# Performance work log

Measured on AMD Instinct MI355X. Metric: run time of the kernel, lower is better.

The kernel has to match this reference:

```python
import jax, jax.numpy as jnp
import numpy as np

B, Z, OUT, NODES = 2048, 64, 512, 64
TRIPLES = 3 * (NODES - 1)  # (self, left, right) per real node
EPS_BN = 1e-5
EPS_TLN = 1e-5
SLOPE = 0.01  # LeakyReLU default


def setup_inputs() -> dict:
    key = jax.random.key(0)
    ks = jax.random.split(key, 12)
    def n(k, shape, s=0.05):
        return jax.random.normal(k, shape, jnp.float32) * s
    inp = {
        "trees": jax.random.normal(ks[0], (B, Z), jnp.float32),
        "indexes": jax.random.randint(ks[1], (B, TRIPLES, 1), 0, NODES),
        # MLP: Linear(Z,64) -> BN -> Linear(64,256) -> BN -> Linear(256,1024) -> BN -> Linear(1024,4096) -> BN
        "w1": n(ks[2], (64, Z)),      "b1": jnp.zeros((64,), jnp.float32),
        "g1": jnp.ones((64,), jnp.float32),   "be1": jnp.zeros((64,), jnp.float32),
        "w2": n(ks[3], (256, 64)),    "b2": jnp.zeros((256,), jnp.float32),
        "g2": jnp.ones((256,), jnp.float32),  "be2": jnp.zeros((256,), jnp.float32),
        "w3": n(ks[4], (1024, 256)),  "b3": jnp.zeros((1024,), jnp.float32),
        "g3": jnp.ones((1024,), jnp.float32), "be3": jnp.zeros((1024,), jnp.float32),
        "w4": n(ks[5], (4096, 1024)), "b4": jnp.zeros((4096,), jnp.float32),
        "g4": jnp.ones((4096,), jnp.float32), "be4": jnp.zeros((4096,), jnp.float32),
        # BinaryTreeConv weights: Conv1d(in,out,kernel=3,stride=3) -> (out,in,3)
        "cw1": n(ks[6], (128, 64, 3)),  "cb1": jnp.zeros((128,), jnp.float32),
        "cw2": n(ks[7], (256, 128, 3)), "cb2": jnp.zeros((256,), jnp.float32),
        "cw3": n(ks[8], (OUT, 256, 3)), "cb3": jnp.zeros((OUT,), jnp.float32),
    }
    return inp


def _bn(x, g, b):
    # BatchNorm1d in training mode: batch statistics, biased variance
    m = jnp.mean(x, axis=0)
    v = jnp.var(x, axis=0)
    return g * (x - m) * jax.lax.rsqrt(v + EPS_BN) + b


def _lrelu(x):
    return jnp.where(x > 0, x, SLOPE * x)


def _tree_conv(x, idx, w, b):
    # x: (B, C, N); idx: (B, 3M) node indices; w: (O, C, 3)
    Bn, C, _ = x.shape
    expanded = jnp.take_along_axis(x, idx[:, None, :], axis=2)  # (B, C, 3M) gather
    expanded = expanded.reshape(Bn, C, -1, 3)                    # (B, C, M, 3)
    out = jnp.einsum('bcmk,ock->bom', expanded, w) + b[None, :, None]
    zero = jnp.zeros((Bn, w.shape[0], 1), x.dtype)               # re-attach null-node slot
    return jnp.concatenate([zero, out], axis=2)                  # (B, O, M+1)


def _tree_norm(x):
    # TreeLayerNorm: normalize over (channels, nodes) per sample; torch.std is unbiased
    m = jnp.mean(x, axis=(1, 2), keepdims=True)
    s = jnp.std(x, axis=(1, 2), ddof=1, keepdims=True)
    return (x - m) / (s + EPS_TLN)


def reference(trees, indexes, w1, b1, g1, be1, w2, b2, g2, be2, w3, b3, g3, be3,
              w4, b4, g4, be4, cw1, cb1, cw2, cb2, cw3, cb3):
    idx = indexes[..., 0]  # (B, 3M)
    h = _lrelu(_bn(trees @ w1.T + b1, g1, be1))
    h = _lrelu(_bn(h @ w2.T + b2, g2, be2))
    h = _lrelu(_bn(h @ w3.T + b3, g3, be3))
    h = _lrelu(_bn(h @ w4.T + b4, g4, be4))
    x = h.reshape(h.shape[0], 64, 64)  # (B, C=64, N=64)
    x = _lrelu(_tree_norm(_tree_conv(x, idx, cw1, cb1)))
    x = _lrelu(_tree_norm(_tree_conv(x, idx, cw2, cb2)))
    x = _lrelu(_tree_norm(_tree_conv(x, idx, cw3, cb3)))
    return x  # (B, OUT, 64)
```

## Files before the change

kernel.cpp:

```cpp
#include <hip/hip_runtime.h>

typedef unsigned short u16;
typedef unsigned int   u32;
typedef __attribute__((ext_vector_type(8))) short short8;
typedef __attribute__((ext_vector_type(4))) float f32x4;
typedef __attribute__((ext_vector_type(4))) u16  u16x4;

#define DI __device__ __forceinline__

DI float b2f(u16 v){ return __builtin_bit_cast(float, (u32)v << 16); }
DI u16 f2b(float f){ u32 u = __builtin_bit_cast(u32, f); return (u16)((u + 0x7fffu + ((u >> 16) & 1u)) >> 16); }
DI float lrelu(float v){ return v > 0.f ? v : 0.01f * v; }

__global__ __launch_bounds__(256)
void cvt_bf16(const float* __restrict__ in, u16* __restrict__ out, int n4)
{
  int i = blockIdx.x*256 + threadIdx.x;
  if (i >= n4) return;
  float4 v = ((const float4*)in)[i];
  u16x4 o; o[0]=f2b(v.x); o[1]=f2b(v.y); o[2]=f2b(v.z); o[3]=f2b(v.w);
  *(u16x4*)(out + (size_t)i*4) = o;
}

template<int BM, int BN, int WROWS, int WCOLS, int RT, int CT, bool APPLY>
__global__ __launch_bounds__(WROWS*WCOLS*64)
void gemm_bn(const float* __restrict__ A, const u16* __restrict__ W,
             const float* __restrict__ ssA,
             float* __restrict__ Y, float* __restrict__ part,
             int M, int N, int K)
{
  constexpr int NT  = WROWS*WCOLS*64;
  constexpr int ALD = (BM*4)/NT;
  constexpr int BLD = (BN*4)/NT;
  __shared__ __align__(16) u16 As[BM*32];
  __shared__ __align__(16) u16 Bs[BN*32];
  __shared__ float colS[WROWS][BN], colS2[WROWS][BN];
  const int tid  = threadIdx.x;
  const int wave = tid >> 6, lane = tid & 63;
  const int wr = wave / WCOLS, wc = wave % WCOLS;
  const int lrow = lane & 15, kg = lane >> 4;
  const int m0 = blockIdx.x * BM, n0 = blockIdx.y * BN;
  f32x4 acc[RT][CT] = {};
  for (int k0 = 0; k0 < K; k0 += 32) {
    uint4 av[ALD], bv[BLD];
#pragma unroll
    for (int i = 0; i < ALD; i++){
      int x = tid + i*NT; int kc = k0 + (x&3)*8;
      const float* ap = A + (size_t)(m0 + (x>>2))*K + kc;
      float4 y0 = *(const float4*)ap, y1 = *(const float4*)(ap + 4);
      float v[8] = {y0.x,y0.y,y0.z,y0.w,y1.x,y1.y,y1.z,y1.w};
      if constexpr (APPLY){
        float4 c0 = *(const float4*)(ssA + kc),     c1 = *(const float4*)(ssA + kc + 4);
        float4 h0 = *(const float4*)(ssA + K + kc), h1 = *(const float4*)(ssA + K + kc + 4);
        v[0]=lrelu(v[0]*c0.x+h0.x); v[1]=lrelu(v[1]*c0.y+h0.y);
        v[2]=lrelu(v[2]*c0.z+h0.z); v[3]=lrelu(v[3]*c0.w+h0.w);
        v[4]=lrelu(v[4]*c1.x+h1.x); v[5]=lrelu(v[5]*c1.y+h1.y);
        v[6]=lrelu(v[6]*c1.z+h1.z); v[7]=lrelu(v[7]*c1.w+h1.w);
      }
      u32 w0 = (u32)f2b(v[0]) | ((u32)f2b(v[1])<<16);
      u32 w1 = (u32)f2b(v[2]) | ((u32)f2b(v[3])<<16);
      u32 w2 = (u32)f2b(v[4]) | ((u32)f2b(v[5])<<16);
      u32 w3 = (u32)f2b(v[6]) | ((u32)f2b(v[7])<<16);
      av[i] = (uint4){w0,w1,w2,w3};
    }
#pragma unroll
    for (int i = 0; i < BLD; i++){ int x = tid + i*NT; bv[i] = *(const uint4*)(W + (size_t)(n0 + (x>>2))*K + k0 + (x&3)*8); }
    __syncthreads();
#pragma unroll
    for (int i = 0; i < ALD; i++){ *(uint4*)(As + (tid + i*NT)*8) = av[i]; }
#pragma unroll
    for (int i = 0; i < BLD; i++){ *(uint4*)(Bs + (tid + i*NT)*8) = bv[i]; }
    __syncthreads();
    short8 af[RT], bfr[CT];
#pragma unroll
    for (int r = 0; r < RT; r++) af[r]  = *(const short8*)(As + ((wr*RT + r)*16 + lrow)*32 + kg*8);
#pragma unroll
    for (int c = 0; c < CT; c++) bfr[c] = *(const short8*)(Bs + ((wc*CT + c)*16 + lrow)*32 + kg*8);
#pragma unroll
    for (int r = 0; r < RT; r++)
#pragma unroll
      for (int c = 0; c < CT; c++)
        acc[r][c] = __builtin_amdgcn_mfma_f32_16x16x32_bf16(af[r], bfr[c], acc[r][c], 0, 0, 0);
  }
#pragma unroll
  for (int r = 0; r < RT; r++)
#pragma unroll
    for (int c = 0; c < CT; c++)
#pragma unroll
      for (int i = 0; i < 4; i++){
        int m = m0 + (wr*RT + r)*16 + kg*4 + i;
        int n = n0 + (wc*CT + c)*16 + lrow;
        Y[(size_t)m*N + n] = acc[r][c][i];
      }
#pragma unroll
  for (int c = 0; c < CT; c++){
    float s = 0.f, s2 = 0.f;
#pragma unroll
    for (int r = 0; r < RT; r++)
#pragma unroll
      for (int i = 0; i < 4; i++){ float v = acc[r][c][i]; s += v; s2 += v*v; }
    s  += __shfl_xor(s, 16);  s  += __shfl_xor(s, 32);
    s2 += __shfl_xor(s2, 16); s2 += __shfl_xor(s2, 32);
    if (kg == 0){ colS[wr][(wc*CT + c)*16 + lrow] = s; colS2[wr][(wc*CT + c)*16 + lrow] = s2; }
  }
  __syncthreads();
  if (tid < BN){
    float S = 0.f, S2 = 0.f;
#pragma unroll
    for (int w = 0; w < WROWS; w++){ S += colS[w][tid]; S2 += colS2[w][tid]; }
    part[(size_t)(blockIdx.x*2+0)*N + n0 + tid] = S;
    part[(size_t)(blockIdx.x*2+1)*N + n0 + tid] = S2;
  }
}

__global__ __launch_bounds__(256)
void bn_finalize(const float* __restrict__ part, const float* __restrict__ g,
                 const float* __restrict__ be, float* __restrict__ ss, int N, int M, int split)
{
  int n = blockIdx.x*256 + threadIdx.x;
  if (n >= N) return;
  float s = 0.f, s2 = 0.f;
  for (int i = 0; i < split; i++){ s += part[(size_t)(i*2+0)*N + n]; s2 += part[(size_t)(i*2+1)*N + n]; }
  float inv  = 1.f / (float)M;
  float mean = s * inv;
  float var  = fmaxf(s2*inv - mean*mean, 0.f);
  float sc   = g[n] * rsqrtf(var + 1e-5f);
  ss[n]     = sc;
  ss[N + n] = be[n] - mean*sc;
}

__global__ __launch_bounds__(256)
void bn_apply4_t(const float* __restrict__ Y, const float* __restrict__ ss, u16* __restrict__ Xt)
{
  const int b = blockIdx.x, tid = threadIdx.x;
  __shared__ u16 t[64*65];
  for (int j = tid; j < 4096; j += 256){
    float v = Y[(size_t)b*4096 + j];
    v = lrelu(v*ss[j] + ss[4096 + j]);
    int c = j >> 6, n = j & 63;
    t[c*65 + n] = f2b(v);
  }
  __syncthreads();
  for (int e = tid; e < 4096; e += 256){
    int n = e >> 6, c = e & 63;
    Xt[(size_t)b*4096 + n*64 + c] = t[c*65 + n];
  }
}

__global__ __launch_bounds__(256)
void repack_w_frag(const float* __restrict__ w, u16* __restrict__ wr, int O, int C, int lgC)
{
  int e = blockIdx.x*256 + threadIdx.x;
  int R = 3*C;
  if (e >= O*R) return;
  int NK   = R >> 5;
  int j    = e & 7;
  int lane = (e >> 3) & 63;
  int blk  = e >> 9;
  int tr   = blk / NK, kb = blk - tr*NK;
  int row  = tr*16 + (lane & 15);
  int kcol = kb*32 + (lane >> 4)*8 + j;
  int k = kcol >> lgC; int c = kcol & (C-1);
  wr[e] = f2b(w[(size_t)row*R + c*3 + k]);
}

template<int C, int O, int WAVES, int MINW, bool PIPE, bool LAST>
__global__ __launch_bounds__(WAVES*64, MINW)
void conv_norm(const u16* __restrict__ Xin, const u16* __restrict__ Wr,
               const float* __restrict__ cb, const int* __restrict__ gidx,
               u16* __restrict__ Xout, float* __restrict__ Outf)
{
  constexpr int R    = 3*C;
  constexpr int NK   = R/32;
  constexpr int CSI  = C + 8;
  constexpr int RT   = O/(WAVES*16);
  constexpr int NT   = WAVES*64;
  constexpr int LGC  = (C==64)?6:((C==128)?7:8);
  constexpr int LG32 = LGC - 5;
  __shared__ __align__(16) u16 xs[65*CSI];
  __shared__ int idxs[192];
  __shared__ float red[2*WAVES];
  const int b = blockIdx.x, tid = threadIdx.x;
  const int wave = tid >> 6, lane = tid & 63;
  const int lrow = lane & 15, kg = lane >> 4;

  const u16* xg = Xin + (size_t)b*64*C;
  for (int e = tid; e < 64*(C/8); e += NT){
    int row = e/(C/8), t = e%(C/8);
    *(uint4*)(xs + row*CSI + t*8) = *(const uint4*)(xg + row*C + t*8);
  }
  for (int e = tid; e < C/8; e += NT){ uint4 z = {0,0,0,0}; *(uint4*)(xs + 64*CSI + e*8) = z; }
  if (tid < 189){ int v = gidx[b*189 + tid]; idxs[tid] = v & 63; }
  __syncthreads();

  int jr0[4], jr1[4], jr2[4];
#pragma unroll
  for (int ct = 0; ct < 4; ct++){
    int n = ct*16 + lrow;
    jr0[ct] = (n == 0) ? 64 : idxs[3*(n-1) + 0];
    jr1[ct] = (n == 0) ? 64 : idxs[3*(n-1) + 1];
    jr2[ct] = (n == 0) ? 64 : idxs[3*(n-1) + 2];
  }

  const u16* wbase = Wr + ((size_t)wave*NK << 9) + lane*8;

  auto loadA = [&](short8* af, int kb32){
#pragma unroll
    for (int r = 0; r < RT; r++)
      af[r] = *(const short8*)(wbase + (((size_t)(WAVES*r)*NK + kb32) << 9));
  };
  auto loadB = [&](short8* bfr, int kb32){
    const int k  = kb32 >> LG32;
    const int c0 = ((kb32*32) & (C-1)) + kg*8;
#pragma unroll
    for (int ct = 0; ct < 4; ct++){
      int row = (k == 0) ? jr0[ct] : ((k == 1) ? jr1[ct] : jr2[ct]);
      bfr[ct] = *(const short8*)(xs + row*CSI + c0);
    }
  };

  f32x4 acc[RT][4] = {};
  auto domfma = [&](short8* af, short8* bfr){
    __builtin_amdgcn_s_setprio(1);
#pragma unroll
    for (int r = 0; r < RT; r++)
#pragma unroll
      for (int ct = 0; ct < 4; ct++)
        acc[r][ct] = __builtin_amdgcn_mfma_f32_16x16x32_bf16(af[r], bfr[ct], acc[r][ct], 0, 0, 0);
    __builtin_amdgcn_s_setprio(0);
  };

  if constexpr (PIPE) {
    short8 afA[RT], bfA[4], afB[RT], bfB[4];
    loadA(afA, 0); loadB(bfA, 0);
    for (int kb32 = 0; kb32 < NK; kb32 += 2){
      loadA(afB, kb32+1); loadB(bfB, kb32+1);
      domfma(afA, bfA);
      if (kb32 + 2 < NK){ loadA(afA, kb32+2); loadB(bfA, kb32+2); }
      domfma(afB, bfB);
    }
  } else {
    for (int kb32 = 0; kb32 < NK; kb32++){
      short8 af[RT], bfr[4];
      loadA(af, kb32); loadB(bfr, kb32);
      domfma(af, bfr);
    }
  }

  float s = 0.f, s2 = 0.f;
#pragma unroll
  for (int r = 0; r < RT; r++)
#pragma unroll
    for (int i = 0; i < 4; i++){
      int o = (wave + WAVES*r)*16 + kg*4 + i;
      float bias = cb[o];
#pragma unroll
      for (int ct = 0; ct < 4; ct++){
        int n = ct*16 + lrow;
        float v = acc[r][ct][i];
        if (n != 0) v += bias;
        acc[r][ct][i] = v;
        s += v; s2 += v*v;
      }
    }
#pragma unroll
  for (int off = 32; off > 0; off >>= 1){ s += __shfl_down(s, off); s2 += __shfl_down(s2, off); }
  if (lane == 0){ red[wave] = s; red[WAVES + wave] = s2; }
  __syncthreads();
  if (tid == 0){
    float S = 0.f, S2 = 0.f;
    for (int w = 0; w < WAVES; w++){ S += red[w]; S2 += red[WAVES + w]; }
    const float NV = (float)(O*64);
    float mean = S / NV;
    float var  = fmaxf(S2/NV - mean*mean, 0.f) * (NV/(NV-1.f));
    float sc   = 1.f / (sqrtf(var) + 1e-5f);
    red[0] = mean; red[1] = sc;
  }
  __syncthreads();
  const float mean = red[0], sc = red[1];

  if constexpr (LAST) {
#pragma unroll
    for (int r = 0; r < RT; r++)
#pragma unroll
      for (int ct = 0; ct < 4; ct++)
#pragma unroll
        for (int i = 0; i < 4; i++){
          int o = (wave + WAVES*r)*16 + kg*4 + i;
          int n = ct*16 + lrow;
          Outf[(size_t)b*(O*64) + o*64 + n] = lrelu((acc[r][ct][i] - mean)*sc);
        }
  } else {
#pragma unroll
    for (int r = 0; r < RT; r++)
#pragma unroll
      for (int ct = 0; ct < 4; ct++){
        int o0 = (wave + WAVES*r)*16 + kg*4;
        int n  = ct*16 + lrow;
        u16x4 pk;
#pragma unroll
        for (int i = 0; i < 4; i++) pk[i] = f2b(lrelu((acc[r][ct][i] - mean)*sc));
        *(u16x4*)(Xout + (size_t)b*64*O + (size_t)n*O + o0) = pk;
      }
  }
}

extern "C" void kernel_launch(void* const* d_in, const int* in_sizes, int n_in,
                              void* d_out, int out_size, void* d_ws, size_t ws_size,
                              hipStream_t stream)
{
  const float* trees = (const float*)d_in[0];
  const int*   gidx  = (const int*)d_in[1];
  const float* w1 = (const float*)d_in[2];
  const float* g1 = (const float*)d_in[4];  const float* be1 = (const float*)d_in[5];
  const float* w2 = (const float*)d_in[6];
  const float* g2 = (const float*)d_in[8];  const float* be2 = (const float*)d_in[9];
  const float* w3 = (const float*)d_in[10];
  const float* g3 = (const float*)d_in[12]; const float* be3 = (const float*)d_in[13];
  const float* w4 = (const float*)d_in[14];
  const float* g4 = (const float*)d_in[16]; const float* be4 = (const float*)d_in[17];
  const float* cw1 = (const float*)d_in[18]; const float* cb1 = (const float*)d_in[19];
  const float* cw2 = (const float*)d_in[20]; const float* cb2 = (const float*)d_in[21];
  const float* cw3 = (const float*)d_in[22]; const float* cb3 = (const float*)d_in[23];

  char* ws = (char*)d_ws;
  size_t off = 0;
  auto alloc = [&](size_t bytes)->char*{ char* p = ws + off; off += (bytes + 255) & ~(size_t)255; return p; };
  u16*   Wr1  = (u16*)  alloc(128*192*2);
  u16*   Wr2  = (u16*)  alloc(256*384*2);
  u16*   Wr3  = (u16*)  alloc(512*768*2);
  float* part = (float*)alloc(64*4096*4);
  float* ss1  = (float*)alloc(2*64*4);
  float* ss2  = (float*)alloc(2*256*4);
  float* ss3  = (float*)alloc(2*1024*4);
  float* ss4  = (float*)alloc(2*4096*4);
  u16*   Xc3  = (u16*)  alloc((size_t)2048*64*256*2);

  u16*   ob   = (u16*)d_out;
  float* outF = (float*)d_out;
  float* Ya   = (float*)ob;
  u16*   Wb1  = ob + 19660800;
  u16*   Wb2  = ob + 19664896;
  u16*   Wb3  = ob + 19681280;
  u16*   Wb4  = ob + 19943424;
  u16*   Xt1  = ob + 25165824;
  u16*   Xc2  = ob + 33554432;
  float* Yb   = (float*)(ob + 50331648);

  cvt_bf16<<<(4096/4+255)/256,   256, 0, stream>>>(w1, Wb1, 4096/4);
  cvt_bf16<<<(16384/4+255)/256,  256, 0, stream>>>(w2, Wb2, 16384/4);
  cvt_bf16<<<(262144/4+255)/256, 256, 0, stream>>>(w3, Wb3, 262144/4);
  cvt_bf16<<<(4194304/4+255)/256,256, 0, stream>>>(w4, Wb4, 4194304/4);

  repack_w_frag<<<(128*192+255)/256, 256, 0, stream>>>(cw1, Wr1, 128, 64, 6);
  repack_w_frag<<<(256*384+255)/256, 256, 0, stream>>>(cw2, Wr2, 256, 128, 7);
  repack_w_frag<<<(512*768+255)/256, 256, 0, stream>>>(cw3, Wr3, 512, 256, 8);

  gemm_bn<64,64,4,1,1,4,false><<<dim3(32,1), 256, 0, stream>>>(trees, Wb1, nullptr, Ya, part, 2048, 64, 64);
  bn_finalize<<<1, 256, 0, stream>>>(part, g1, be1, ss1, 64, 2048, 32);
  gemm_bn<64,64,4,1,1,4,true ><<<dim3(32,4), 256, 0, stream>>>(Ya, Wb2, ss1, Yb, part, 2048, 256, 64);
  bn_finalize<<<1, 256, 0, stream>>>(part, g2, be2, ss2, 256, 2048, 32);
  gemm_bn<64,64,4,1,1,4,true ><<<dim3(32,16), 256, 0, stream>>>(Yb, Wb3, ss2, Ya, part, 2048, 1024, 256);
  bn_finalize<<<4, 256, 0, stream>>>(part, g3, be3, ss3, 1024, 2048, 32);
  gemm_bn<128,128,2,2,4,4,true><<<dim3(16,32), 256, 0, stream>>>(Ya, Wb4, ss3, Yb, part, 2048, 4096, 1024);
  bn_finalize<<<16, 256, 0, stream>>>(part, g4, be4, ss4, 4096, 2048, 16);
  bn_apply4_t<<<2048, 256, 0, stream>>>(Yb, ss4, Xt1);

  conv_norm< 64,128,8,4,true ,false><<<2048, 512, 0, stream>>>(Xt1, Wr1, cb1, gidx, Xc2, nullptr);
  conv_norm<128,256,8,4,true ,false><<<2048, 512, 0, stream>>>(Xc2, Wr2, cb2, gidx, Xc3, nullptr);
  conv_norm<256,512,8,4,false,true ><<<2048, 512, 0, stream>>>(Xc3, Wr3, cb3, gidx, nullptr, outF);
}
```

Measured before the change: 360.1 us.

## Fuse BN finalize into GEMMs, BN apply into first conv, merge prep kernels

Merges the four weight-conversion launches into one kernel and the three conv-weight repacks into another. Each BN-finalize step (layers 1-3) is recomputed per block inside the next GEMM's prologue into shared memory. The final BN apply and transpose is folded into the first tree-conv's shared-memory load, so the Xt1 intermediate is no longer written or read. This removes about eight launches and one full activation round trip, at the cost of redundant per-block reduction of partial sums and strided LDS writes in the first conv.

```diff
diff --git a/kernel.cpp b/kernel.cpp
--- a/kernel.cpp
+++ b/kernel.cpp
@@ -13,20 +13,55 @@
 DI float lrelu(float v){ return v > 0.f ? v : 0.01f * v; }
 
 __global__ __launch_bounds__(256)
-void cvt_bf16(const float* __restrict__ in, u16* __restrict__ out, int n4)
+void cvt_w_all(const float* __restrict__ w1, u16* __restrict__ d1,
+               const float* __restrict__ w2, u16* __restrict__ d2,
+               const float* __restrict__ w3, u16* __restrict__ d3,
+               const float* __restrict__ w4, u16* __restrict__ d4)
 {
   int i = blockIdx.x*256 + threadIdx.x;
-  if (i >= n4) return;
-  float4 v = ((const float4*)in)[i];
+  const float* s; u16* d; int li;
+  if      (i < 1024)   { s = w1; d = d1; li = i; }
+  else if (i < 5120)   { s = w2; d = d2; li = i - 1024; }
+  else if (i < 70656)  { s = w3; d = d3; li = i - 5120; }
+  else if (i < 1119232){ s = w4; d = d4; li = i - 70656; }
+  else return;
+  float4 v = ((const float4*)s)[li];
   u16x4 o; o[0]=f2b(v.x); o[1]=f2b(v.y); o[2]=f2b(v.z); o[3]=f2b(v.w);
-  *(u16x4*)(out + (size_t)i*4) = o;
+  *(u16x4*)(d + (size_t)li*4) = o;
+}
+
+DI void repack_one(const float* __restrict__ w, u16* __restrict__ wr,
+                   int e, int C, int lgC)
+{
+  int R = 3*C;
+  int NK   = R >> 5;
+  int j    = e & 7;
+  int lane = (e >> 3) & 63;
+  int blk  = e >> 9;
+  int tr   = blk / NK, kb = blk - tr*NK;
+  int row  = tr*16 + (lane & 15);
+  int kcol = kb*32 + (lane >> 4)*8 + j;
+  int k = kcol >> lgC; int c = kcol & (C-1);
+  wr[e] = f2b(w[(size_t)row*R + c*3 + k]);
+}
+
+__global__ __launch_bounds__(256)
+void repack_all(const float* __restrict__ c1, u16* __restrict__ r1,
+                const float* __restrict__ c2, u16* __restrict__ r2,
+                const float* __restrict__ c3, u16* __restrict__ r3)
+{
+  int i = blockIdx.x*256 + threadIdx.x;
+  if      (i < 24576)  repack_one(c1, r1, i,          64, 6);
+  else if (i < 122880) repack_one(c2, r2, i - 24576, 128, 7);
+  else if (i < 516096) repack_one(c3, r3, i - 122880,256, 8);
 }
 
 template<int BM, int BN, int WROWS, int WCOLS, int RT, int CT, bool APPLY>
 __global__ __launch_bounds__(WROWS*WCOLS*64)
 void gemm_bn(const float* __restrict__ A, const u16* __restrict__ W,
-             const float* __restrict__ ssA,
-             float* __restrict__ Y, float* __restrict__ part,
+             const float* __restrict__ partIn, const float* __restrict__ gA,
+             const float* __restrict__ beA, int splitIn,
+             float* __restrict__ Y, float* __restrict__ partOut,
              int M, int N, int K)
 {
   constexpr int NT  = WROWS*WCOLS*64;
@@ -35,11 +70,30 @@
   __shared__ __align__(16) u16 As[BM*32];
   __shared__ __align__(16) u16 Bs[BN*32];
   __shared__ float colS[WROWS][BN], colS2[WROWS][BN];
+  __shared__ __align__(16) float ssL[APPLY ? 2048 : 4];
   const int tid  = threadIdx.x;
   const int wave = tid >> 6, lane = tid & 63;
   const int wr = wave / WCOLS, wc = wave % WCOLS;
   const int lrow = lane & 15, kg = lane >> 4;
   const int m0 = blockIdx.x * BM, n0 = blockIdx.y * BN;
+
+  if constexpr (APPLY){
+    for (int n = tid; n < K; n += NT){
+      float s = 0.f, s2 = 0.f;
+      for (int i = 0; i < splitIn; i++){
+        s  += partIn[(size_t)(i*2+0)*K + n];
+        s2 += partIn[(size_t)(i*2+1)*K + n];
+      }
+      float inv  = 1.f / (float)M;
+      float mean = s * inv;
+      float var  = fmaxf(s2*inv - mean*mean, 0.f);
+      float sc   = gA[n] * rsqrtf(var + 1e-5f);
+      ssL[n]     = sc;
+      ssL[K + n] = beA[n] - mean*sc;
+    }
+    __syncthreads();
+  }
+
   f32x4 acc[RT][CT] = {};
   for (int k0 = 0; k0 < K; k0 += 32) {
     uint4 av[ALD], bv[BLD];
@@ -50,8 +104,8 @@
       float4 y0 = *(const float4*)ap, y1 = *(const float4*)(ap + 4);
       float v[8] = {y0.x,y0.y,y0.z,y0.w,y1.x,y1.y,y1.z,y1.w};
       if constexpr (APPLY){
-        float4 c0 = *(const float4*)(ssA + kc),     c1 = *(const float4*)(ssA + kc + 4);
-        float4 h0 = *(const float4*)(ssA + K + kc), h1 = *(const float4*)(ssA + K + kc + 4);
+        float4 c0 = *(const float4*)(ssL + kc),     c1 = *(const float4*)(ssL + kc + 4);
+        float4 h0 = *(const float4*)(ssL + K + kc), h1 = *(const float4*)(ssL + K + kc + 4);
         v[0]=lrelu(v[0]*c0.x+h0.x); v[1]=lrelu(v[1]*c0.y+h0.y);
         v[2]=lrelu(v[2]*c0.z+h0.z); v[3]=lrelu(v[3]*c0.w+h0.w);
         v[4]=lrelu(v[4]*c1.x+h1.x); v[5]=lrelu(v[5]*c1.y+h1.y);
@@ -108,8 +162,8 @@
     float S = 0.f, S2 = 0.f;
 #pragma unroll
     for (int w = 0; w < WROWS; w++){ S += colS[w][tid]; S2 += colS2[w][tid]; }
-    part[(size_t)(blockIdx.x*2+0)*N + n0 + tid] = S;
-    part[(size_t)(blockIdx.x*2+1)*N + n0 + tid] = S2;
+    partOut[(size_t)(blockIdx.x*2+0)*N + n0 + tid] = S;
+    partOut[(size_t)(blockIdx.x*2+1)*N + n0 + tid] = S2;
   }
 }
 
@@ -129,44 +183,11 @@
   ss[N + n] = be[n] - mean*sc;
 }
 
-__global__ __launch_bounds__(256)
-void bn_apply4_t(const float* __restrict__ Y, const float* __restrict__ ss, u16* __restrict__ Xt)
-{
-  const int b = blockIdx.x, tid = threadIdx.x;
-  __shared__ u16 t[64*65];
-  for (int j = tid; j < 4096; j += 256){
-    float v = Y[(size_t)b*4096 + j];
-    v = lrelu(v*ss[j] + ss[4096 + j]);
-    int c = j >> 6, n = j & 63;
-    t[c*65 + n] = f2b(v);
-  }
-  __syncthreads();
-  for (int e = tid; e < 4096; e += 256){
-    int n = e >> 6, c = e & 63;
-    Xt[(size_t)b*4096 + n*64 + c] = t[c*65 + n];
-  }
-}
-
-__global__ __launch_bounds__(256)
-void repack_w_frag(const float* __restrict__ w, u16* __restrict__ wr, int O, int C, int lgC)
-{
-  int e = blockIdx.x*256 + threadIdx.x;
-  int R = 3*C;
-  if (e >= O*R) return;
-  int NK   = R >> 5;
-  int j    = e & 7;
-  int lane = (e >> 3) & 63;
-  int blk  = e >> 9;
-  int tr   = blk / NK, kb = blk - tr*NK;
-  int row  = tr*16 + (lane & 15);
-  int kcol = kb*32 + (lane >> 4)*8 + j;
-  int k = kcol >> lgC; int c = kcol & (C-1);
-  wr[e] = f2b(w[(size_t)row*R + c*3 + k]);
-}
-
-template<int C, int O, int WAVES, int MINW, bool PIPE, bool LAST>
+template<int C, int O, int WAVES, int MINW, bool PIPE, bool LAST, bool FIRST>
 __global__ __launch_bounds__(WAVES*64, MINW)
-void conv_norm(const u16* __restrict__ Xin, const u16* __restrict__ Wr,
+void conv_norm(const u16* __restrict__ Xin, const float* __restrict__ XinF,
+               const float* __restrict__ ssA,
+               const u16* __restrict__ Wr,
                const float* __restrict__ cb, const int* __restrict__ gidx,
                u16* __restrict__ Xout, float* __restrict__ Outf)
 {
@@ -184,10 +205,31 @@
   const int wave = tid >> 6, lane = tid & 63;
   const int lrow = lane & 15, kg = lane >> 4;
 
-  const u16* xg = Xin + (size_t)b*64*C;
-  for (int e = tid; e < 64*(C/8); e += NT){
-    int row = e/(C/8), t = e%(C/8);
-    *(uint4*)(xs + row*CSI + t*8) = *(const uint4*)(xg + row*C + t*8);
+  if constexpr (FIRST){
+    const float* yg = XinF + (size_t)b*4096;
+    int j0 = tid*8;
+    float4 a0 = *(const float4*)(yg + j0);
+    float4 a1 = *(const float4*)(yg + j0 + 4);
+    float4 s0 = *(const float4*)(ssA + j0);
+    float4 s1 = *(const float4*)(ssA + j0 + 4);
+    float4 h0 = *(const float4*)(ssA + 4096 + j0);
+    float4 h1 = *(const float4*)(ssA + 4096 + j0 + 4);
+    int c = j0 >> 6, n0 = j0 & 63;
+    u16* xp = xs + c;
+    xp[(n0+0)*CSI] = f2b(lrelu(a0.x*s0.x + h0.x));
+    xp[(n0+1)*CSI] = f2b(lrelu(a0.y*s0.y + h0.y));
+    xp[(n0+2)*CSI] = f2b(lrelu(a0.z*s0.z + h0.z));
+    xp[(n0+3)*CSI] = f2b(lrelu(a0.w*s0.w + h0.w));
+    xp[(n0+4)*CSI] = f2b(lrelu(a1.x*s1.x + h1.x));
+    xp[(n0+5)*CSI] = f2b(lrelu(a1.y*s1.y + h1.y));
+    xp[(n0+6)*CSI] = f2b(lrelu(a1.z*s1.z + h1.z));
+    xp[(n0+7)*CSI] = f2b(lrelu(a1.w*s1.w + h1.w));
+  } else {
+    const u16* xg = Xin + (size_t)b*64*C;
+    for (int e = tid; e < 64*(C/8); e += NT){
+      int row = e/(C/8), t = e%(C/8);
+      *(uint4*)(xs + row*CSI + t*8) = *(const uint4*)(xg + row*C + t*8);
+    }
   }
   for (int e = tid; e < C/8; e += NT){ uint4 z = {0,0,0,0}; *(uint4*)(xs + 64*CSI + e*8) = z; }
   if (tid < 189){ int v = gidx[b*189 + tid]; idxs[tid] = v & 63; }
@@ -326,15 +368,13 @@
   char* ws = (char*)d_ws;
   size_t off = 0;
   auto alloc = [&](size_t bytes)->char*{ char* p = ws + off; off += (bytes + 255) & ~(size_t)255; return p; };
-  u16*   Wr1  = (u16*)  alloc(128*192*2);
-  u16*   Wr2  = (u16*)  alloc(256*384*2);
-  u16*   Wr3  = (u16*)  alloc(512*768*2);
-  float* part = (float*)alloc(64*4096*4);
-  float* ss1  = (float*)alloc(2*64*4);
-  float* ss2  = (float*)alloc(2*256*4);
-  float* ss3  = (float*)alloc(2*1024*4);
-  float* ss4  = (float*)alloc(2*4096*4);
-  u16*   Xc3  = (u16*)  alloc((size_t)2048*64*256*2);
+  u16*   Wr1   = (u16*)  alloc(128*192*2);
+  u16*   Wr2   = (u16*)  alloc(256*384*2);
+  u16*   Wr3   = (u16*)  alloc(512*768*2);
+  float* partA = (float*)alloc(64*4096*4);
+  float* partB = (float*)alloc(64*4096*4);
+  float* ss4   = (float*)alloc(2*4096*4);
+  u16*   Xc3   = (u16*)  alloc((size_t)2048*64*256*2);
 
   u16*   ob   = (u16*)d_out;
   float* outF = (float*)d_out;
@@ -343,30 +383,19 @@
   u16*   Wb2  = ob + 19664896;
   u16*   Wb3  = ob + 19681280;
   u16*   Wb4  = ob + 19943424;
-  u16*   Xt1  = ob + 25165824;
   u16*   Xc2  = ob + 33554432;
   float* Yb   = (float*)(ob + 50331648);
 
-  cvt_bf16<<<(4096/4+255)/256,   256, 0, stream>>>(w1, Wb1, 4096/4);
-  cvt_bf16<<<(16384/4+255)/256,  256, 0, stream>>>(w2, Wb2, 16384/4);
-  cvt_bf16<<<(262144/4+255)/256, 256, 0, stream>>>(w3, Wb3, 262144/4);
-  cvt_bf16<<<(4194304/4+255)/256,256, 0, stream>>>(w4, Wb4, 4194304/4);
-
-  repack_w_frag<<<(128*192+255)/256, 256, 0, stream>>>(cw1, Wr1, 128, 64, 6);
-  repack_w_frag<<<(256*384+255)/256, 256, 0, stream>>>(cw2, Wr2, 256, 128, 7);
-  repack_w_frag<<<(512*768+255)/256, 256, 0, stream>>>(cw3, Wr3, 512, 256, 8);
-
-  gemm_bn<64,64,4,1,1,4,false><<<dim3(32,1), 256, 0, stream>>>(trees, Wb1, nullptr, Ya, part, 2048, 64, 64);
-  bn_finalize<<<1, 256, 0, stream>>>(part, g1, be1, ss1, 64, 2048, 32);
-  gemm_bn<64,64,4,1,1,4,true ><<<dim3(32,4), 256, 0, stream>>>(Ya, Wb2, ss1, Yb, part, 2048, 256, 64);
-  bn_finalize<<<1, 256, 0, stream>>>(part, g2, be2, ss2, 256, 2048, 32);
-  gemm_bn<64,64,4,1,1,4,true ><<<dim3(32,16), 256, 0, stream>>>(Yb, Wb3, ss2, Ya, part, 2048, 1024, 256);
-  bn_finalize<<<4, 256, 0, stream>>>(part, g3, be3, ss3, 1024, 2048, 32);
-  gemm_bn<128,128,2,2,4,4,true><<<dim3(16,32), 256, 0, stream>>>(Ya, Wb4, ss3, Yb, part, 2048, 4096, 1024);
-  bn_finalize<<<16, 256, 0, stream>>>(part, g4, be4, ss4, 4096, 2048, 16);
-  bn_apply4_t<<<2048, 256, 0, stream>>>(Yb, ss4, Xt1);
-
-  conv_norm< 64,128,8,4,true ,false><<<2048, 512, 0, stream>>>(Xt1, Wr1, cb1, gidx, Xc2, nullptr);
-  conv_norm<128,256,8,4,true ,false><<<2048, 512, 0, stream>>>(Xc2, Wr2, cb2, gidx, Xc3, nullptr);
-  conv_norm<256,512,8,4,false,true ><<<2048, 512, 0, stream>>>(Xc3, Wr3, cb3, gidx, nullptr, outF);
-}
+  cvt_w_all <<<4372, 256, 0, stream>>>(w1, Wb1, w2, Wb2, w3, Wb3, w4, Wb4);
+  repack_all<<<2016, 256, 0, stream>>>(cw1, Wr1, cw2, Wr2, cw3, Wr3);
+
+  gemm_bn<64,64,4,1,1,4,false><<<dim3(32,1),  256, 0, stream>>>(trees, Wb1, nullptr, nullptr, nullptr, 0,  Ya, partA, 2048, 64,   64);
+  gemm_bn<64,64,4,1,1,4,true ><<<dim3(32,4),  256, 0, stream>>>(Ya,    Wb2, partA,   g1,      be1,     32, Yb, partB, 2048, 256,  64);
+  gemm_bn<64,64,4,1,1,4,true ><<<dim3(32,16), 256, 0, stream>>>(Yb,    Wb3, partB,   g2,      be2,     32, Ya, partA, 2048, 1024, 256);
+  gemm_bn<128,128,2,2,4,4,true><<<dim3(16,32),256, 0, stream>>>(Ya,    Wb4, partA,   g3,      be3,     32, Yb, partB, 2048, 4096, 1024);
+  bn_finalize<<<16, 256, 0, stream>>>(partB, g4, be4, ss4, 4096, 2048, 16);
+
+  conv_norm< 64,128,8,4,true ,false,true ><<<2048, 512, 0, stream>>>(nullptr, Yb, ss4, Wr1, cb1, gidx, Xc2, nullptr);
+  conv_norm<128,256,8,4,true ,false,false><<<2048, 512, 0, stream>>>(Xc2, nullptr, nullptr, Wr2, cb2, gidx, Xc3, nullptr);
+  conv_norm<256,512,8,4,false,true ,false><<<2048, 512, 0, stream>>>(Xc3, nullptr, nullptr, Wr3, cb3, gidx, nullptr, outF);
+}
```

Result: faster. 350.0 us (-2.8%).
